# Kernel optimization log

Measured on AMD Instinct MI355X. Metric: run time of the kernel, lower is better.

Reference implementation:

```python
import jax, jax.numpy as jnp
import numpy as np

B, S, E, H, D = 64, 512, 512, 8, 64  # batch, n_steps, embedding_size, head_count, QKV_dim

def setup_inputs() -> dict:
    key = jax.random.key(0)
    ks = jax.random.split(key, 7)
    x = jax.random.normal(ks[0], (B, S, E), dtype=jnp.float32)
    mask = jax.random.randint(ks[1], (B, S), 0, 2).astype(jnp.float32)  # 1 = masked out
    WQ = jax.random.normal(ks[2], (H, E, D), dtype=jnp.float32) * 0.1
    WK = jax.random.normal(ks[3], (H, E, D), dtype=jnp.float32) * 0.1
    WV = jax.random.normal(ks[4], (H, E, D), dtype=jnp.float32) * 0.1
    BE = jax.random.normal(ks[5], (S, E), dtype=jnp.float32) * 0.1
    WO = jax.random.normal(ks[6], (H * D, E), dtype=jnp.float32) * 0.1
    return {"x": x, "mask": mask, "WQ": WQ, "WK": WK, "WV": WV, "BE": BE, "WO": WO}

def reference(x, mask, WQ, WK, WV, BE, WO):
    # add learned positional bias
    h = x + BE  # [B,S,E]
    # per-head projections, vectorized over heads
    Q = jnp.einsum('bse,hed->bhsd', h, WQ)
    K = jnp.einsum('bse,hed->bhsd', h, WK)
    V = jnp.einsum('bse,hed->bhsd', h, WV)
    # NOTE: original scales by sqrt(embedding_size), not sqrt(QKV_dim)
    scores = jnp.einsum('bhsd,bhtd->bhst', Q, K) / np.sqrt(E).astype(np.float32)
    # additive mask trick: mask tiled over query dim, key positions masked where mask==1
    scores = scores - mask[:, None, None, :] * 1e10
    alpha = jax.nn.softmax(scores, axis=-1)  # [B,H,S,S]
    attn = jnp.einsum('bhst,bhtd->bhsd', alpha, V)  # [B,H,S,D]
    # concat heads along feature dim -> [B,S,H*D], then output projection
    attn = jnp.transpose(attn, (0, 2, 1, 3)).reshape(x.shape[0], x.shape[1], -1)
    return attn @ WO  # [B,S,E]
```

## Files before the change

### kernel.cpp

```cpp
#include <hip/hip_runtime.h>
#include <hip/hip_bf16.h>


#define Bn 64
#define Sn 512
#define En 512
#define Hn 8
#define Dn 64

typedef __attribute__((ext_vector_type(8))) short s8v;
typedef __attribute__((ext_vector_type(4))) float f4v;

__device__ __forceinline__ unsigned short f2bf(float f) {
    union { float f; unsigned int u; } v; v.f = f;
    unsigned int u = v.u;
    u += 0x7fffu + ((u >> 16) & 1u);
    return (unsigned short)(u >> 16);
}

__device__ __forceinline__ void async16(const unsigned short* g, unsigned short* l) {
    __builtin_amdgcn_global_load_lds((const __attribute__((address_space(1))) void*)g,
                                     (__attribute__((address_space(3))) void*)l, 16, 0, 0);
}
__device__ __forceinline__ void async4(const float* g, float* l) {
    __builtin_amdgcn_global_load_lds((const __attribute__((address_space(1))) void*)g,
                                     (__attribute__((address_space(3))) void*)l, 4, 0, 0);
}

__global__ __launch_bounds__(256) void prep_h(const float* __restrict__ x,
                                              const float* __restrict__ BE,
                                              unsigned short* __restrict__ hbf) {
    int i = (blockIdx.x * 256 + threadIdx.x) * 4;
    int se = i % (Sn * En);
    float4 a = *(const float4*)(x + i);
    float4 b = *(const float4*)(BE + se);
    ushort4 o;
    o.x = f2bf(a.x + b.x); o.y = f2bf(a.y + b.y);
    o.z = f2bf(a.z + b.z); o.w = f2bf(a.w + b.w);
    *(ushort4*)(hbf + i) = o;
}

__global__ __launch_bounds__(256) void prep_w(const float* __restrict__ WQ,
                                              const float* __restrict__ WK,
                                              const float* __restrict__ WV,
                                              const float* __restrict__ WO,
                                              unsigned short* __restrict__ Wqkvt,
                                              unsigned short* __restrict__ WOt) {
    int idx = blockIdx.x * 256 + threadIdx.x;
    const int NW = 3 * Hn * Dn * En;
    if (idx < NW) {
        int e = idx & 511;
        int d = (idx >> 9) & 63;
        int h = (idx >> 15) & 7;
        int m = idx >> 18;
        const float* W = (m == 0) ? WQ : (m == 1) ? WK : WV;
        Wqkvt[idx] = f2bf(W[(h * En + e) * Dn + d]);
    } else {
        int j = idx - NW;
        int n = j & 511;
        int e = j >> 9;
        WOt[j] = f2bf(WO[n * En + e]);
    }
}

__global__ __launch_bounds__(256) void qkv_gemm(const unsigned short* __restrict__ hbf,
                                                const unsigned short* __restrict__ Wqkvt,
                                                unsigned short* __restrict__ Qo,
                                                unsigned short* __restrict__ Ko,
                                                unsigned short* __restrict__ Vt) {
    int nb = blockIdx.x, mb = blockIdx.y;
    __shared__ __align__(16) unsigned short At[128 * 64];
    __shared__ __align__(16) unsigned short Bt[128 * 64];
    int tid = threadIdx.x;
    int w = tid >> 6, lane = tid & 63, quad = lane >> 4, l16 = lane & 15;
    int wr = w >> 1, wc = w & 1;
    int lrow = lane >> 3;
    int lseg = ((lane & 7) ^ lrow) * 8;

    f4v acc[4][4];
#pragma unroll
    for (int i = 0; i < 4; i++)
#pragma unroll
        for (int n = 0; n < 4; n++) acc[i][n] = (f4v){0.f, 0.f, 0.f, 0.f};

    const unsigned short* Ag = hbf + (size_t)mb * 128 * 512;
    const unsigned short* Bg = Wqkvt + (size_t)nb * 128 * 512;

    for (int kc = 0; kc < 8; kc++) {
        __syncthreads();
#pragma unroll
        for (int i = 0; i < 4; i++) {
            int r0 = w * 32 + i * 8;
            async16(Ag + (r0 + lrow) * 512 + kc * 64 + lseg, &At[r0 * 64]);
            async16(Bg + (r0 + lrow) * 512 + kc * 64 + lseg, &Bt[r0 * 64]);
        }
        __syncthreads();
#pragma unroll
        for (int ks = 0; ks < 2; ks++) {
            int sw = ((ks * 4 + quad) ^ (l16 & 7)) * 8;
            s8v a[4], b[4];
#pragma unroll
            for (int i = 0; i < 4; i++)
                a[i] = *(const s8v*)&At[(wr * 64 + i * 16 + l16) * 64 + sw];
#pragma unroll
            for (int n = 0; n < 4; n++)
                b[n] = *(const s8v*)&Bt[(wc * 64 + n * 16 + l16) * 64 + sw];
#pragma unroll
            for (int i = 0; i < 4; i++)
#pragma unroll
                for (int n = 0; n < 4; n++)
                    acc[i][n] = __builtin_amdgcn_mfma_f32_16x16x32_bf16(a[i], b[n], acc[i][n], 0, 0, 0);
        }
    }

    int mat = nb >> 2;
    int h = (nb & 3) * 2 + wc;
    int b = mb >> 2;
    int s0 = (mb & 3) * 128 + wr * 64;
    const float qscale = 0.04419417382415922f;

    if (mat < 2) {
        unsigned short* op = (mat == 0) ? Qo : Ko;
        float sc = (mat == 0) ? qscale : 1.0f;
#pragma unroll
        for (int i = 0; i < 4; i++)
#pragma unroll
            for (int n = 0; n < 4; n++)
#pragma unroll
                for (int r = 0; r < 4; r++) {
                    int s = s0 + i * 16 + quad * 4 + r;
                    int d = n * 16 + l16;
                    op[(size_t)((b * Hn + h) * Sn + s) * Dn + d] = f2bf(acc[i][n][r] * sc);
                }
    } else {
#pragma unroll
        for (int i = 0; i < 4; i++)
#pragma unroll
            for (int n = 0; n < 4; n++) {
                int d = n * 16 + l16;
                int s = s0 + i * 16 + quad * 4;
                ushort4 pk;
                pk.x = f2bf(acc[i][n][0]); pk.y = f2bf(acc[i][n][1]);
                pk.z = f2bf(acc[i][n][2]); pk.w = f2bf(acc[i][n][3]);
                *(ushort4*)&Vt[(size_t)((b * Hn + h) * Dn + d) * Sn + s] = pk;
            }
    }
}

__global__ __launch_bounds__(256) void attn_kernel(const unsigned short* __restrict__ Q,
                                                   const unsigned short* __restrict__ K,
                                                   const unsigned short* __restrict__ Vt,
                                                   const float* __restrict__ mask,
                                                   unsigned short* __restrict__ attn) {
    int qt = blockIdx.x, h = blockIdx.y, b = blockIdx.z;
    __shared__ __align__(16) unsigned short Qs[64 * 64];
    __shared__ __align__(16) unsigned short Ks[64 * 64];
    __shared__ __align__(16) unsigned short Vts[64 * 64];
    __shared__ __align__(16) unsigned short Ps[4][16 * 64];
    __shared__ float maskv[64];
    int tid = threadIdx.x;
    int w = tid >> 6, lane = tid & 63, quad = lane >> 4, l16 = lane & 15;
    int lrow = lane >> 3;
    int lseg = ((lane & 7) ^ lrow) * 8;
    int l7 = l16 & 7, lh = l16 >> 3;
    int q4 = (quad & 1) * 4;

    const unsigned short* Qg = Q + (size_t)((b * Hn + h) * Sn + qt * 64) * Dn;
    const unsigned short* Kg = K + (size_t)((b * Hn + h) * Sn) * Dn;
    const unsigned short* Vg = Vt + (size_t)((b * Hn + h) * Dn) * Sn;

#pragma unroll
    for (int i = 0; i < 2; i++) {
        int r0 = w * 16 + i * 8;
        async16(Qg + (r0 + lrow) * 64 + lseg, &Qs[r0 * 64]);
    }

    float psum[4] = {0.f, 0.f, 0.f, 0.f};
    f4v Oacc[4];
#pragma unroll
    for (int n = 0; n < 4; n++) Oacc[n] = (f4v){0.f, 0.f, 0.f, 0.f};

    for (int tt = 0; tt < 8; tt++) {
        __syncthreads();
#pragma unroll
        for (int i = 0; i < 2; i++) {
            int r0 = w * 16 + i * 8;
            async16(Kg + (tt * 64 + r0 + lrow) * 64 + lseg, &Ks[r0 * 64]);
            async16(Vg + (r0 + lrow) * Sn + tt * 64 + lseg, &Vts[r0 * 64]);
        }
        if (w == 0) async4(mask + b * Sn + tt * 64 + lane, maskv);
        __syncthreads();

        f4v sacc[4];
#pragma unroll
        for (int n = 0; n < 4; n++) sacc[n] = (f4v){0.f, 0.f, 0.f, 0.f};
#pragma unroll
        for (int ks = 0; ks < 2; ks++) {
            int sw = ((ks * 4 + quad) ^ l7) * 8;
            s8v aq = *(const s8v*)&Qs[(w * 16 + l16) * 64 + sw];
#pragma unroll
            for (int n = 0; n < 4; n++) {
                s8v bk = *(const s8v*)&Ks[(n * 16 + l16) * 64 + sw];
                sacc[n] = __builtin_amdgcn_mfma_f32_16x16x32_bf16(aq, bk, sacc[n], 0, 0, 0);
            }
        }

        unsigned short* Pw = Ps[w];
#pragma unroll
        for (int n = 0; n < 4; n++) {
            float msub = maskv[n * 16 + l16] * -1e10f;
            int colpart = n * 2 + lh;
#pragma unroll
            for (int r = 0; r < 4; r++) {
                float p = __expf(sacc[n][r] + msub);
                unsigned int u = __float_as_uint(p);
                psum[r] += __uint_as_float(u & 0xffff0000u);
                int row = quad * 4 + r;
                Pw[row * 64 + ((colpart ^ (q4 + r)) * 8) + l7] = (unsigned short)(u >> 16);
            }
        }

#pragma unroll
        for (int ks = 0; ks < 2; ks++) {
            int sw = ((ks * 4 + quad) ^ l7) * 8;
            s8v ap = *(const s8v*)&Pw[l16 * 64 + ((ks * 4 + quad) ^ l7) * 8];
#pragma unroll
            for (int n = 0; n < 4; n++) {
                s8v bv = *(const s8v*)&Vts[(n * 16 + l16) * 64 + sw];
                Oacc[n] = __builtin_amdgcn_mfma_f32_16x16x32_bf16(ap, bv, Oacc[n], 0, 0, 0);
            }
        }
    }

#pragma unroll
    for (int off = 1; off < 16; off <<= 1)
#pragma unroll
        for (int r = 0; r < 4; r++) psum[r] += __shfl_xor(psum[r], off, 64);
    float inv[4];
#pragma unroll
    for (int r = 0; r < 4; r++) inv[r] = 1.0f / psum[r];

#pragma unroll
    for (int n = 0; n < 4; n++)
#pragma unroll
        for (int r = 0; r < 4; r++) {
            int srow = qt * 64 + w * 16 + quad * 4 + r;
            int col = h * 64 + n * 16 + l16;
            attn[(size_t)(b * Sn + srow) * (Hn * Dn) + col] = f2bf(Oacc[n][r] * inv[r]);
        }
}

__global__ __launch_bounds__(256) void outproj(const unsigned short* __restrict__ attn,
                                               const unsigned short* __restrict__ WOt,
                                               float* __restrict__ out) {
    int nb = blockIdx.x, mb = blockIdx.y;
    __shared__ __align__(16) unsigned short At[128 * 64];
    __shared__ __align__(16) unsigned short Bt[128 * 64];
    int tid = threadIdx.x;
    int w = tid >> 6, lane = tid & 63, quad = lane >> 4, l16 = lane & 15;
    int wr = w >> 1, wc = w & 1;
    int lrow = lane >> 3;
    int lseg = ((lane & 7) ^ lrow) * 8;

    f4v acc[4][4];
#pragma unroll
    for (int i = 0; i < 4; i++)
#pragma unroll
        for (int n = 0; n < 4; n++) acc[i][n] = (f4v){0.f, 0.f, 0.f, 0.f};

    const unsigned short* Ag = attn + (size_t)mb * 128 * 512;
    const unsigned short* Bg = WOt + (size_t)nb * 128 * 512;

    for (int kc = 0; kc < 8; kc++) {
        __syncthreads();
#pragma unroll
        for (int i = 0; i < 4; i++) {
            int r0 = w * 32 + i * 8;
            async16(Ag + (r0 + lrow) * 512 + kc * 64 + lseg, &At[r0 * 64]);
            async16(Bg + (r0 + lrow) * 512 + kc * 64 + lseg, &Bt[r0 * 64]);
        }
        __syncthreads();
#pragma unroll
        for (int ks = 0; ks < 2; ks++) {
            int sw = ((ks * 4 + quad) ^ (l16 & 7)) * 8;
            s8v a[4], b[4];
#pragma unroll
            for (int i = 0; i < 4; i++)
                a[i] = *(const s8v*)&At[(wr * 64 + i * 16 + l16) * 64 + sw];
#pragma unroll
            for (int n = 0; n < 4; n++)
                b[n] = *(const s8v*)&Bt[(wc * 64 + n * 16 + l16) * 64 + sw];
#pragma unroll
            for (int i = 0; i < 4; i++)
#pragma unroll
                for (int n = 0; n < 4; n++)
                    acc[i][n] = __builtin_amdgcn_mfma_f32_16x16x32_bf16(a[i], b[n], acc[i][n], 0, 0, 0);
        }
    }
#pragma unroll
    for (int i = 0; i < 4; i++)
#pragma unroll
        for (int n = 0; n < 4; n++)
#pragma unroll
            for (int r = 0; r < 4; r++) {
                int row = mb * 128 + wr * 64 + i * 16 + quad * 4 + r;
                int col = nb * 128 + wc * 64 + n * 16 + l16;
                out[(size_t)row * 512 + col] = acc[i][n][r];
            }
}

extern "C" void kernel_launch(void* const* d_in, const int* in_sizes, int n_in,
                              void* d_out, int out_size, void* d_ws, size_t ws_size,
                              hipStream_t stream) {
    const float* x    = (const float*)d_in[0];
    const float* mask = (const float*)d_in[1];
    const float* WQ   = (const float*)d_in[2];
    const float* WK   = (const float*)d_in[3];
    const float* WV   = (const float*)d_in[4];
    const float* BE   = (const float*)d_in[5];
    const float* WO   = (const float*)d_in[6];
    float* out = (float*)d_out;

    char* ws = (char*)d_ws;
    unsigned short* hbf   = (unsigned short*)(ws);
    unsigned short* Wqkvt = (unsigned short*)(ws + 33554432);
    unsigned short* WOt   = (unsigned short*)(ws + 35127296);
    unsigned short* Qp    = (unsigned short*)(ws + 35651584);
    unsigned short* Kp    = (unsigned short*)(ws + 69206016);
    unsigned short* Vtp   = (unsigned short*)(ws + 102760448);
    unsigned short* attnp = (unsigned short*)(ws + 136314880);

    prep_h<<<16384, 256, 0, stream>>>(x, BE, hbf);
    prep_w<<<4096, 256, 0, stream>>>(WQ, WK, WV, WO, Wqkvt, WOt);
    qkv_gemm<<<dim3(12, 256), 256, 0, stream>>>(hbf, Wqkvt, Qp, Kp, Vtp);
    attn_kernel<<<dim3(Sn / 64, Hn, Bn), 256, 0, stream>>>(Qp, Kp, Vtp, mask, attnp);
    outproj<<<dim3(4, 256), 256, 0, stream>>>(attnp, WOt, out);
}
```

Baseline: 326.3 us.

## Process all queries per (batch,head) block to reuse K/V tiles across 512 queries

The attention kernel now launches one 512-thread block per (batch, head). Each of its 8 waves keeps 64 query rows in registers, so every K/V tile is loaded once and reused by all 512 queries instead of being reloaded for each 64-query tile. The scale is folded with log2(e) so exp2f can replace __expf. This cuts global K/V traffic, but it also cuts the grid to 512 blocks, raises register pressure (aq plus a 4x4 accumulator array), and still has no double-buffering of tile loads.

```diff
diff --git a/kernel.cpp b/kernel.cpp
--- a/kernel.cpp
+++ b/kernel.cpp
@@ -117,7 +117,7 @@
     int h = (nb & 3) * 2 + wc;
     int b = mb >> 2;
     int s0 = (mb & 3) * 128 + wr * 64;
-    const float qscale = 0.04419417382415922f;
+    const float qscale = 0.06375873f;
 
     if (mat < 2) {
         unsigned short* op = (mat == 0) ? Qo : Ko;
@@ -147,107 +147,115 @@
     }
 }
 
-__global__ __launch_bounds__(256) void attn_kernel(const unsigned short* __restrict__ Q,
+__global__ __launch_bounds__(512) void attn_kernel(const unsigned short* __restrict__ Q,
                                                    const unsigned short* __restrict__ K,
                                                    const unsigned short* __restrict__ Vt,
                                                    const float* __restrict__ mask,
                                                    unsigned short* __restrict__ attn) {
-    int qt = blockIdx.x, h = blockIdx.y, b = blockIdx.z;
-    __shared__ __align__(16) unsigned short Qs[64 * 64];
-    __shared__ __align__(16) unsigned short Ks[64 * 64];
-    __shared__ __align__(16) unsigned short Vts[64 * 64];
-    __shared__ __align__(16) unsigned short Ps[4][16 * 64];
+    int bh = blockIdx.x;
+    int h = bh & 7, b = bh >> 3;
+    __shared__ __align__(16) unsigned short Kc[64 * 64];
+    __shared__ __align__(16) unsigned short Vc[64 * 64];
+    __shared__ __align__(16) unsigned short Ps[8][16 * 64];
     __shared__ float maskv[64];
     int tid = threadIdx.x;
     int w = tid >> 6, lane = tid & 63, quad = lane >> 4, l16 = lane & 15;
-    int lrow = lane >> 3;
-    int lseg = ((lane & 7) ^ lrow) * 8;
     int l7 = l16 & 7, lh = l16 >> 3;
     int q4 = (quad & 1) * 4;
 
-    const unsigned short* Qg = Q + (size_t)((b * Hn + h) * Sn + qt * 64) * Dn;
-    const unsigned short* Kg = K + (size_t)((b * Hn + h) * Sn) * Dn;
-    const unsigned short* Vg = Vt + (size_t)((b * Hn + h) * Dn) * Sn;
-
-#pragma unroll
-    for (int i = 0; i < 2; i++) {
-        int r0 = w * 16 + i * 8;
-        async16(Qg + (r0 + lrow) * 64 + lseg, &Qs[r0 * 64]);
-    }
-
-    float psum[4] = {0.f, 0.f, 0.f, 0.f};
-    f4v Oacc[4];
-#pragma unroll
-    for (int n = 0; n < 4; n++) Oacc[n] = (f4v){0.f, 0.f, 0.f, 0.f};
-
-    for (int tt = 0; tt < 8; tt++) {
-        __syncthreads();
-#pragma unroll
-        for (int i = 0; i < 2; i++) {
-            int r0 = w * 16 + i * 8;
-            async16(Kg + (tt * 64 + r0 + lrow) * 64 + lseg, &Ks[r0 * 64]);
-            async16(Vg + (r0 + lrow) * Sn + tt * 64 + lseg, &Vts[r0 * 64]);
-        }
-        if (w == 0) async4(mask + b * Sn + tt * 64 + lane, maskv);
-        __syncthreads();
-
-        f4v sacc[4];
-#pragma unroll
-        for (int n = 0; n < 4; n++) sacc[n] = (f4v){0.f, 0.f, 0.f, 0.f};
-#pragma unroll
-        for (int ks = 0; ks < 2; ks++) {
-            int sw = ((ks * 4 + quad) ^ l7) * 8;
-            s8v aq = *(const s8v*)&Qs[(w * 16 + l16) * 64 + sw];
+    const unsigned short* Qg = Q + (size_t)(bh * Sn) * Dn;
+    const unsigned short* Kg = K + (size_t)(bh * Sn) * Dn;
+    const unsigned short* Vg = Vt + (size_t)(bh * Dn) * Sn;
+
+    s8v aq[4][2];
+#pragma unroll
+    for (int i = 0; i < 4; i++)
+#pragma unroll
+        for (int ks = 0; ks < 2; ks++)
+            aq[i][ks] = *(const s8v*)&Qg[((w * 4 + i) * 16 + l16) * 64 + ks * 32 + quad * 8];
+
+    f4v acc[4][4];
+    float psum[4][4];
+#pragma unroll
+    for (int i = 0; i < 4; i++)
+#pragma unroll
+        for (int n = 0; n < 4; n++) {
+            acc[i][n] = (f4v){0.f, 0.f, 0.f, 0.f};
+            psum[i][n] = 0.f;
+        }
+
+    int srow = w * 8 + (lane >> 3);
+    int sseg = ((lane & 7) ^ (srow & 7)) * 8;
+    unsigned short* kdst = &Kc[w * 512];
+    unsigned short* vdst = &Vc[w * 512];
+
+    for (int kc = 0; kc < 8; kc++) {
+        __syncthreads();
+        async16(Kg + (kc * 64 + srow) * 64 + sseg, kdst);
+        async16(Vg + srow * 512 + kc * 64 + sseg, vdst);
+        if (w == 0) async4(mask + b * Sn + kc * 64 + lane, maskv);
+        __syncthreads();
+
+        unsigned short* Pw = Ps[w];
+#pragma unroll
+        for (int i = 0; i < 4; i++) {
+            f4v sacc[4];
+#pragma unroll
+            for (int n = 0; n < 4; n++) sacc[n] = (f4v){0.f, 0.f, 0.f, 0.f};
+#pragma unroll
+            for (int ks = 0; ks < 2; ks++) {
+                int sw = ((ks * 4 + quad) ^ l7) * 8;
+#pragma unroll
+                for (int n = 0; n < 4; n++) {
+                    s8v bk = *(const s8v*)&Kc[(n * 16 + l16) * 64 + sw];
+                    sacc[n] = __builtin_amdgcn_mfma_f32_16x16x32_bf16(aq[i][ks], bk, sacc[n], 0, 0, 0);
+                }
+            }
 #pragma unroll
             for (int n = 0; n < 4; n++) {
-                s8v bk = *(const s8v*)&Ks[(n * 16 + l16) * 64 + sw];
-                sacc[n] = __builtin_amdgcn_mfma_f32_16x16x32_bf16(aq, bk, sacc[n], 0, 0, 0);
-            }
-        }
-
-        unsigned short* Pw = Ps[w];
-#pragma unroll
-        for (int n = 0; n < 4; n++) {
-            float msub = maskv[n * 16 + l16] * -1e10f;
-            int colpart = n * 2 + lh;
+                float msub = maskv[n * 16 + l16] * -1.4426950409e10f;
+                int colpart = n * 2 + lh;
+#pragma unroll
+                for (int r = 0; r < 4; r++) {
+                    float p = exp2f(sacc[n][r] + msub);
+                    unsigned int u = __float_as_uint(p);
+                    psum[i][r] += __uint_as_float(u & 0xffff0000u);
+                    Pw[(quad * 4 + r) * 64 + ((colpart ^ (q4 + r)) * 8) + l7] =
+                        (unsigned short)(u >> 16);
+                }
+            }
+#pragma unroll
+            for (int ks = 0; ks < 2; ks++) {
+                int sw = ((ks * 4 + quad) ^ l7) * 8;
+                s8v ap = *(const s8v*)&Pw[l16 * 64 + sw];
+#pragma unroll
+                for (int n = 0; n < 4; n++) {
+                    s8v bv = *(const s8v*)&Vc[(n * 16 + l16) * 64 + sw];
+                    acc[i][n] = __builtin_amdgcn_mfma_f32_16x16x32_bf16(ap, bv, acc[i][n], 0, 0, 0);
+                }
+            }
+        }
+    }
+
+#pragma unroll
+    for (int i = 0; i < 4; i++) {
+        float inv[4];
+#pragma unroll
+        for (int r = 0; r < 4; r++) {
+            float s = psum[i][r];
+#pragma unroll
+            for (int off = 1; off < 16; off <<= 1) s += __shfl_xor(s, off, 64);
+            inv[r] = 1.0f / s;
+        }
+#pragma unroll
+        for (int n = 0; n < 4; n++)
 #pragma unroll
             for (int r = 0; r < 4; r++) {
-                float p = __expf(sacc[n][r] + msub);
-                unsigned int u = __float_as_uint(p);
-                psum[r] += __uint_as_float(u & 0xffff0000u);
-                int row = quad * 4 + r;
-                Pw[row * 64 + ((colpart ^ (q4 + r)) * 8) + l7] = (unsigned short)(u >> 16);
-            }
-        }
-
-#pragma unroll
-        for (int ks = 0; ks < 2; ks++) {
-            int sw = ((ks * 4 + quad) ^ l7) * 8;
-            s8v ap = *(const s8v*)&Pw[l16 * 64 + ((ks * 4 + quad) ^ l7) * 8];
-#pragma unroll
-            for (int n = 0; n < 4; n++) {
-                s8v bv = *(const s8v*)&Vts[(n * 16 + l16) * 64 + sw];
-                Oacc[n] = __builtin_amdgcn_mfma_f32_16x16x32_bf16(ap, bv, Oacc[n], 0, 0, 0);
-            }
-        }
-    }
-
-#pragma unroll
-    for (int off = 1; off < 16; off <<= 1)
-#pragma unroll
-        for (int r = 0; r < 4; r++) psum[r] += __shfl_xor(psum[r], off, 64);
-    float inv[4];
-#pragma unroll
-    for (int r = 0; r < 4; r++) inv[r] = 1.0f / psum[r];
-
-#pragma unroll
-    for (int n = 0; n < 4; n++)
-#pragma unroll
-        for (int r = 0; r < 4; r++) {
-            int srow = qt * 64 + w * 16 + quad * 4 + r;
-            int col = h * 64 + n * 16 + l16;
-            attn[(size_t)(b * Sn + srow) * (Hn * Dn) + col] = f2bf(Oacc[n][r] * inv[r]);
-        }
+                int query = (w * 4 + i) * 16 + quad * 4 + r;
+                int col = h * 64 + n * 16 + l16;
+                attn[(size_t)(b * Sn + query) * (Hn * Dn) + col] = f2bf(acc[i][n][r] * inv[r]);
+            }
+    }
 }
 
 __global__ __launch_bounds__(256) void outproj(const unsigned short* __restrict__ attn,
@@ -333,6 +341,6 @@
     prep_h<<<16384, 256, 0, stream>>>(x, BE, hbf);
     prep_w<<<4096, 256, 0, stream>>>(WQ, WK, WV, WO, Wqkvt, WOt);
     qkv_gemm<<<dim3(12, 256), 256, 0, stream>>>(hbf, Wqkvt, Qp, Kp, Vtp);
-    attn_kernel<<<dim3(Sn / 64, Hn, Bn), 256, 0, stream>>>(Qp, Kp, Vtp, mask, attnp);
+    attn_kernel<<<Bn * Hn, 512, 0, stream>>>(Qp, Kp, Vtp, mask, attnp);
     outproj<<<dim3(4, 256), 256, 0, stream>>>(attnp, WOt, out);
 }
```

New measurement: 327.7 us. About the same (+0.4%).
